# Kernel optimization log

Measured on AMD Instinct MI355X. Metric: run time of the kernel, lower is better.

## Reference

```python
import jax, jax.numpy as jnp
import numpy as np

M, H, D, P = 256, 32, 128, 4096
N = H * D
L = P + M  # total cache length after concat


def setup_inputs() -> dict:
    key = jax.random.key(0)
    ks = jax.random.split(key, 8)
    X = jax.random.normal(ks[0], (M, N), dtype=jnp.float32)
    # projection weights (nn.Linear stores [out, in]; y = x @ W.T)
    Wq = jax.random.normal(ks[1], (N, N), dtype=jnp.float32) * 0.005
    Wk = jax.random.normal(ks[2], (N, N), dtype=jnp.float32) * 0.005
    Wv = jax.random.normal(ks[3], (N, N), dtype=jnp.float32) * 0.005
    cache_K = jax.random.normal(ks[4], (H, P, D), dtype=jnp.float32) * 0.3
    cache_V = jax.random.normal(ks[5], (H, P, D), dtype=jnp.float32) * 0.3
    noise = jax.random.normal(ks[6], (H, M, L), dtype=jnp.float32) * 0.5
    tau = jnp.asarray(2.0, dtype=jnp.float32)
    return {"X": X, "Wq": Wq, "Wk": Wk, "Wv": Wv,
            "cache_K": cache_K, "cache_V": cache_V, "tau": tau, "noise": noise}


def reference(X, Wq, Wk, Wv, cache_K, cache_V, tau, noise):
    # project and split heads: [M, N] -> [H, M, D]
    q = (X @ Wq.T).reshape(M, H, D).transpose(1, 0, 2)
    k = (X @ Wk.T).reshape(M, H, D).transpose(1, 0, 2)
    v = (X @ Wv.T).reshape(M, H, D).transpose(1, 0, 2)
    k_cache = jnp.concatenate([cache_K, k], axis=1)  # [H, L, D]
    v_cache = jnp.concatenate([cache_V, v], axis=1)  # [H, L, D]
    c = jnp.einsum('hmd,hld->hml', q, k_cache)       # [H, M, L]
    # faithful to source: plain exp normalization (no max-subtract), twice
    c_exp = jnp.exp(c)
    c_exp_perturb = jnp.exp((c + noise) / tau)
    c_div = c_exp / jnp.sum(c_exp, axis=2, keepdims=True)
    c_div_perturb = c_exp_perturb / jnp.sum(c_exp_perturb, axis=2, keepdims=True)
    c_out = jnp.sum(c_div_perturb, axis=1)           # [H, L] token scores
    o = jnp.einsum('hml,hld->hmd', c_div, v_cache)   # [H, M, D]
    o2 = o.transpose(1, 0, 2).reshape(M, N)
    return o2, c_out
```

## Files before the change

kernel.cpp:

```cpp
#include <hip/hip_runtime.h>
#include <hip/hip_bf16.h>

#define MM 256
#define HH 32
#define DD 128
#define PP 4096
#define NN 4096
#define LL 4352
#define NSTR 8
#define SPL 4

typedef __attribute__((ext_vector_type(8))) short short8;
typedef __attribute__((ext_vector_type(4))) float f32x4;

__device__ __forceinline__ unsigned short f2bf(float f) {
    union { float f; unsigned u; } x; x.f = f;
    unsigned u = x.u;
    return (unsigned short)((u + 0x7fffu + ((u >> 16) & 1u)) >> 16);
}

__device__ __forceinline__ float bf2f(unsigned short u) {
    union { unsigned u; float f; } x; x.u = ((unsigned)u) << 16;
    return x.f;
}

__device__ __forceinline__ f32x4 mfma16(short8 a, short8 b, f32x4 c) {
    return __builtin_amdgcn_mfma_f32_16x16x32_bf16(a, b, c, 0, 0, 0);
}

__global__ __launch_bounds__(256) void conv_x_kernel(const float* __restrict__ src,
                                                     unsigned short* __restrict__ dst) {
    int i = blockIdx.x * 256 + threadIdx.x;
    long in0 = (long)i * 8;
    float4 f0 = *(const float4*)(src + in0);
    float4 f1 = *(const float4*)(src + in0 + 4);
    short8 v;
    v[0] = (short)f2bf(f0.x); v[1] = (short)f2bf(f0.y); v[2] = (short)f2bf(f0.z); v[3] = (short)f2bf(f0.w);
    v[4] = (short)f2bf(f1.x); v[5] = (short)f2bf(f1.y); v[6] = (short)f2bf(f1.z); v[7] = (short)f2bf(f1.w);
    *(short8*)(dst + in0) = v;
}

__global__ __launch_bounds__(256) void conv_k_kernel(const float* __restrict__ src,
                                                     unsigned short* __restrict__ dst) {
    int i = blockIdx.x * 256 + threadIdx.x;
    int h = i >> 16;
    long in0 = (long)i * 8;
    float4 f0 = *(const float4*)(src + in0);
    float4 f1 = *(const float4*)(src + in0 + 4);
    short8 v;
    v[0] = (short)f2bf(f0.x); v[1] = (short)f2bf(f0.y); v[2] = (short)f2bf(f0.z); v[3] = (short)f2bf(f0.w);
    v[4] = (short)f2bf(f1.x); v[5] = (short)f2bf(f1.y); v[6] = (short)f2bf(f1.z); v[7] = (short)f2bf(f1.w);
    *(short8*)(dst + in0 + (long)h * (LL - PP) * DD) = v;
}

__global__ __launch_bounds__(256) void conv_vt_kernel(const float* __restrict__ src,
                                                      unsigned short* __restrict__ dst) {
    __shared__ unsigned short tile[64][65];
    int h = blockIdx.z, l0 = blockIdx.x * 64, d0 = blockIdx.y * 64;
    int t = threadIdx.x;
    int r = t >> 2, c0 = (t & 3) * 16;
    const float* sp = src + ((long)h * PP + l0 + r) * DD + d0 + c0;
#pragma unroll
    for (int j = 0; j < 16; j += 4) {
        float4 f = *(const float4*)(sp + j);
        tile[r][c0 + j + 0] = f2bf(f.x); tile[r][c0 + j + 1] = f2bf(f.y);
        tile[r][c0 + j + 2] = f2bf(f.z); tile[r][c0 + j + 3] = f2bf(f.w);
    }
    __syncthreads();
    unsigned short* dp = dst + ((long)h * DD + d0 + r) * LL + l0 + c0;
    short8 o0, o1;
#pragma unroll
    for (int j = 0; j < 8; ++j) o0[j] = (short)tile[c0 + j][r];
#pragma unroll
    for (int j = 0; j < 8; ++j) o1[j] = (short)tile[c0 + 8 + j][r];
    *(short8*)(dp) = o0;
    *(short8*)(dp + 8) = o1;
}

__device__ __forceinline__ void proj_body(unsigned short* As, unsigned short* Bs,
    const unsigned short* __restrict__ xp, const float* __restrict__ wp,
    int& k0, bool guard, short8 (&ar)[4], float4& b0, float4& b1,
    int arow, int ak0, int brow, int bk0, int mo, int no, int lg, int li,
    f32x4 (&acc)[4][2]) {
#pragma unroll
    for (int c = 0; c < 4; ++c) {
        int kb = (ak0 + c * 8) * 2;
        *(short8*)((char*)As + arow * 128 + (kb ^ ((arow & 7) << 4))) = ar[c];
    }
    {
        short8 v;
        v[0] = (short)f2bf(b0.x); v[1] = (short)f2bf(b0.y); v[2] = (short)f2bf(b0.z); v[3] = (short)f2bf(b0.w);
        v[4] = (short)f2bf(b1.x); v[5] = (short)f2bf(b1.y); v[6] = (short)f2bf(b1.z); v[7] = (short)f2bf(b1.w);
        int kb = bk0 * 2;
        *(short8*)((char*)Bs + brow * 128 + (kb ^ ((brow & 7) << 4))) = v;
    }
    __syncthreads();
    if (guard) {
#pragma unroll
        for (int c = 0; c < 4; ++c) ar[c] = *(const short8*)(xp + k0 + 128 + c * 8);
        b0 = *(const float4*)(wp + k0 + 128);
        b1 = *(const float4*)(wp + k0 + 132);
    }
#pragma unroll
    for (int kk = 0; kk < 2; ++kk) {
        short8 a[4], b[2];
        int kb = kk * 64 + lg * 16;
#pragma unroll
        for (int i = 0; i < 4; ++i) {
            int row = mo + i * 16 + li;
            a[i] = *(const short8*)((char*)As + row * 128 + (kb ^ ((row & 7) << 4)));
        }
#pragma unroll
        for (int j = 0; j < 2; ++j) {
            int row = no + j * 16 + li;
            b[j] = *(const short8*)((char*)Bs + row * 128 + (kb ^ ((row & 7) << 4)));
        }
#pragma unroll
        for (int i = 0; i < 4; ++i)
#pragma unroll
            for (int j = 0; j < 2; ++j)
                acc[i][j] = mfma16(a[i], b[j], acc[i][j]);
    }
    __syncthreads();
    k0 += 64;
}

__global__ __launch_bounds__(512) void proj_gemm_kernel(const unsigned short* __restrict__ xb,
    const float* __restrict__ Wq, const float* __restrict__ Wk, const float* __restrict__ Wv,
    float* __restrict__ qkvfP) {
    const int widx = blockIdx.z;
    const float* __restrict__ W = (widx == 0) ? Wq : (widx == 1 ? Wk : Wv);
    const int n0 = blockIdx.x * 64;
    const int ks = blockIdx.y;
    __shared__ unsigned short As[256 * 64];
    __shared__ unsigned short Bs[64 * 64];
    const int t = threadIdx.x;
    const int wv = t >> 6, lane = t & 63;
    const int lg = lane >> 4, li = lane & 15;
    const int mo = (wv >> 1) * 64, no = (wv & 1) * 32;
    f32x4 acc[4][2];
#pragma unroll
    for (int i = 0; i < 4; ++i)
#pragma unroll
        for (int j = 0; j < 2; ++j) acc[i][j] = (f32x4){0.f, 0.f, 0.f, 0.f};

    const int arow = t >> 1, ak0 = (t & 1) * 32;
    const int brow = t >> 3, bk0 = (t & 7) * 8;
    const unsigned short* xp = xb + (long)arow * NN + ak0;
    const float* wp = W + (long)(n0 + brow) * NN + bk0;

    int k0 = ks * 1024;
    short8 aA[4], aB[4];
    float4 bA0, bA1, bB0, bB1;
#pragma unroll
    for (int c = 0; c < 4; ++c) aA[c] = *(const short8*)(xp + k0 + c * 8);
    bA0 = *(const float4*)(wp + k0);
    bA1 = *(const float4*)(wp + k0 + 4);
#pragma unroll
    for (int c = 0; c < 4; ++c) aB[c] = *(const short8*)(xp + k0 + 64 + c * 8);
    bB0 = *(const float4*)(wp + k0 + 64);
    bB1 = *(const float4*)(wp + k0 + 68);

    for (int it2 = 0; it2 < 8; ++it2) {
        const bool guard = (it2 < 7);
        proj_body(As, Bs, xp, wp, k0, guard, aA, bA0, bA1,
                  arow, ak0, brow, bk0, mo, no, lg, li, acc);
        proj_body(As, Bs, xp, wp, k0, guard, aB, bB0, bB1,
                  arow, ak0, brow, bk0, mo, no, lg, li, acc);
    }

    float* dst = qkvfP + ((long)ks * 3 + widx) * MM * NN;
#pragma unroll
    for (int i = 0; i < 4; ++i)
#pragma unroll
        for (int j = 0; j < 2; ++j)
#pragma unroll
            for (int r = 0; r < 4; ++r) {
                int m = mo + i * 16 + lg * 4 + r;
                int n = n0 + no + j * 16 + li;
                dst[(long)m * NN + n] = acc[i][j][r];
            }
}

__global__ __launch_bounds__(256) void epi_qk_kernel(const float* __restrict__ qkvfP,
    unsigned short* __restrict__ qb, unsigned short* __restrict__ kcat) {
    int i = blockIdx.x * 256 + threadIdx.x;
    int w = i >> 17;
    int r = i & 131071;
    int m = r >> 9;
    int n = (r & 511) * 8;
    float4 f0 = {0,0,0,0}, f1 = {0,0,0,0};
#pragma unroll
    for (int s = 0; s < SPL; ++s) {
        const float* sp = qkvfP + ((long)s * 3 + w) * MM * NN + (long)m * NN + n;
        float4 a0 = *(const float4*)(sp);
        float4 a1 = *(const float4*)(sp + 4);
        f0.x += a0.x; f0.y += a0.y; f0.z += a0.z; f0.w += a0.w;
        f1.x += a1.x; f1.y += a1.y; f1.z += a1.z; f1.w += a1.w;
    }
    short8 v;
    v[0]=(short)f2bf(f0.x); v[1]=(short)f2bf(f0.y); v[2]=(short)f2bf(f0.z); v[3]=(short)f2bf(f0.w);
    v[4]=(short)f2bf(f1.x); v[5]=(short)f2bf(f1.y); v[6]=(short)f2bf(f1.z); v[7]=(short)f2bf(f1.w);
    int h = n >> 7, d = n & 127;
    if (w == 0) *(short8*)(qb + ((long)h * MM + m) * DD + d) = v;
    else        *(short8*)(kcat + ((long)h * LL + PP + m) * DD + d) = v;
}

__global__ __launch_bounds__(256) void epi_v_kernel(const float* __restrict__ qkvfP,
    unsigned short* __restrict__ vT) {
    __shared__ unsigned short tile[64][65];
    int m0 = blockIdx.x * 64, n0 = blockIdx.y * 64;
    int t = threadIdx.x;
    int r = t >> 2, c0 = (t & 3) * 16;
#pragma unroll
    for (int j = 0; j < 16; j += 4) {
        float4 f = {0,0,0,0};
#pragma unroll
        for (int s = 0; s < SPL; ++s) {
            const float* sp = qkvfP + ((long)s * 3 + 2) * MM * NN + (long)(m0 + r) * NN + n0 + c0 + j;
            float4 a = *(const float4*)(sp);
            f.x += a.x; f.y += a.y; f.z += a.z; f.w += a.w;
        }
        tile[r][c0 + j + 0] = f2bf(f.x); tile[r][c0 + j + 1] = f2bf(f.y);
        tile[r][c0 + j + 2] = f2bf(f.z); tile[r][c0 + j + 3] = f2bf(f.w);
    }
    __syncthreads();
    int h = n0 >> 7, d0 = n0 & 127;
    unsigned short* dp = vT + ((long)h * DD + d0 + r) * LL + PP + m0 + c0;
    short8 o0, o1;
#pragma unroll
    for (int j = 0; j < 8; ++j) o0[j] = (short)tile[c0 + j][r];
#pragma unroll
    for (int j = 0; j < 8; ++j) o1[j] = (short)tile[c0 + 8 + j][r];
    *(short8*)(dp) = o0;
    *(short8*)(dp + 8) = o1;
}

__global__ __launch_bounds__(256) void attn_score_kernel(const unsigned short* __restrict__ qb,
    const unsigned short* __restrict__ kcat, const float* __restrict__ noise,
    const float* __restrict__ tau, float* __restrict__ S1, float* __restrict__ S2,
    unsigned short* __restrict__ e1b, unsigned short* __restrict__ e2b) {
    const int bid = blockIdx.x;
    const int swz = (bid & 7) * 272 + (bid >> 3);
    const int ls = swz % 17;
    const int mb = (swz / 17) & 3;
    const int h  = swz / 68;
    const int t = threadIdx.x, wv = t >> 6, lane = t & 63;
    const int lg = lane >> 4, li = lane & 15;
    __shared__ unsigned short kbuf[2][32][136];
    __shared__ float cs[64][36];
    const float inv_tau = 1.0f / tau[0];

    const int mA = mb * 64 + wv * 16 + li;
    const unsigned short* qp = qb + ((long)h * MM + mA) * DD + lg * 8;
    short8 aq[4];
#pragma unroll
    for (int dc = 0; dc < 4; ++dc) aq[dc] = *(const short8*)(qp + dc * 32);

    const int row_l = t >> 2;
    const int col0 = (t & 3) * 8;
    const int mrow_g = mb * 64 + row_l;
    const float* np = noise + ((long)h * MM + mrow_g) * LL + ls * 256 + col0;
    unsigned short* e1p = e1b + ((long)h * MM + mrow_g) * LL + ls * 256 + col0;
    unsigned short* e2p = e2b + ((long)h * MM + mrow_g) * LL + ls * 256 + col0;

    const int srow = t >> 3;
    const int scol = (t & 7) * 16;
    const unsigned short* ksrc = kcat + ((long)h * LL + ls * 256 + srow) * DD + scol;

    short8 s0 = *(const short8*)(ksrc);
    short8 s1 = *(const short8*)(ksrc + 8);
    *(short8*)(&kbuf[0][srow][scol]) = s0;
    *(short8*)(&kbuf[0][srow][scol + 8]) = s1;

    float4 nA0 = *(const float4*)(np);
    float4 nA1 = *(const float4*)(np + 4);
    float4 nB0 = *(const float4*)(np + 32);
    float4 nB1 = *(const float4*)(np + 36);

    float s1t = 0.f, s2t = 0.f;
    int cur = 0;
    __syncthreads();

    for (int lc = 0; lc < 8; ++lc) {
        if (lc < 7) {
            const unsigned short* p = ksrc + (long)((lc + 1) * 32) * DD;
            s0 = *(const short8*)(p);
            s1 = *(const short8*)(p + 8);
        }
        f32x4 c0 = (f32x4){0.f,0.f,0.f,0.f}, c1 = (f32x4){0.f,0.f,0.f,0.f};
#pragma unroll
        for (int dc = 0; dc < 4; ++dc) {
            short8 k0 = *(const short8*)(&kbuf[cur][li][dc * 32 + lg * 8]);
            short8 k1 = *(const short8*)(&kbuf[cur][16 + li][dc * 32 + lg * 8]);
            c0 = mfma16(aq[dc], k0, c0);
            c1 = mfma16(aq[dc], k1, c1);
        }
#pragma unroll
        for (int r = 0; r < 4; ++r) {
            cs[wv * 16 + lg * 4 + r][li] = c0[r];
            cs[wv * 16 + lg * 4 + r][16 + li] = c1[r];
        }
        float4 cva = *(const float4*)(&cs[row_l][col0]);
        float4 cvb = *(const float4*)(&cs[row_l][col0 + 4]);
        float cv[8] = {cva.x, cva.y, cva.z, cva.w, cvb.x, cvb.y, cvb.z, cvb.w};
        float nn[8] = {nA0.x, nA0.y, nA0.z, nA0.w, nA1.x, nA1.y, nA1.z, nA1.w};
        short8 v1, v2;
#pragma unroll
        for (int j = 0; j < 8; ++j) {
            float e1 = __expf(cv[j]);
            float e2 = __expf((cv[j] + nn[j]) * inv_tau);
            s1t += e1;
            s2t += e2;
            v1[j] = (short)f2bf(e1);
            v2[j] = (short)f2bf(e2);
        }
        *(short8*)(e1p + lc * 32) = v1;
        *(short8*)(e2p + lc * 32) = v2;
        nA0 = nB0; nA1 = nB1;
        int nx = (lc + 2 < 8) ? (lc + 2) : 7;
        nB0 = *(const float4*)(np + nx * 32);
        nB1 = *(const float4*)(np + nx * 32 + 4);
        if (lc < 7) {
            *(short8*)(&kbuf[cur ^ 1][srow][scol]) = s0;
            *(short8*)(&kbuf[cur ^ 1][srow][scol + 8]) = s1;
        }
        __syncthreads();
        cur ^= 1;
    }

    s1t += __shfl_xor(s1t, 1); s1t += __shfl_xor(s1t, 2);
    s2t += __shfl_xor(s2t, 1); s2t += __shfl_xor(s2t, 2);
    if ((t & 3) == 0) {
        atomicAdd(&S1[h * MM + mrow_g], s1t);
        atomicAdd(&S2[h * MM + mrow_g], s2t);
    }
}

__global__ __launch_bounds__(256) void attn_pv_kernel(const unsigned short* __restrict__ e1b,
    const unsigned short* __restrict__ vT, float* __restrict__ owsP) {
    const int bid = blockIdx.x;
    const int swz = (bid & 7) * 256 + (bid >> 3);
    const int ls = swz & 7;
    const int mb = (swz >> 3) & 3;
    const int dh = (swz >> 5) & 1;
    const int h  = swz >> 6;
    const int t = threadIdx.x, wv = t >> 6, lane = t & 63;
    const int lg = lane >> 4, li = lane & 15;
    __shared__ unsigned short vbuf[2][64][40];
    f32x4 acc[4];
#pragma unroll
    for (int df = 0; df < 4; ++df) acc[df] = (f32x4){0.f, 0.f, 0.f, 0.f};

    const unsigned short* pap = e1b + ((long)h * MM + mb * 64 + wv * 16 + li) * LL + ls * 544 + lg * 8;
    const int vrow = t >> 2, vcol = (t & 3) * 8;
    const unsigned short* vsrc = vT + ((long)h * DD + dh * 64 + vrow) * LL + ls * 544 + vcol;

    short8 vs = *(const short8*)(vsrc);
    *(short8*)(&vbuf[0][vrow][vcol]) = vs;
    short8 pa = __builtin_nontemporal_load((const short8*)(pap));
    int cur = 0;
    __syncthreads();

    for (int lc = 0; lc < 17; ++lc) {
        short8 pan;
        if (lc < 16) {
            vs = *(const short8*)(vsrc + (lc + 1) * 32);
            pan = __builtin_nontemporal_load((const short8*)(pap + (lc + 1) * 32));
        }
#pragma unroll
        for (int df = 0; df < 4; ++df) {
            short8 bv = *(const short8*)(&vbuf[cur][df * 16 + li][lg * 8]);
            acc[df] = mfma16(pa, bv, acc[df]);
        }
        if (lc < 16) {
            *(short8*)(&vbuf[cur ^ 1][vrow][vcol]) = vs;
            pa = pan;
        }
        __syncthreads();
        cur ^= 1;
    }

    const int mD = mb * 64 + wv * 16 + lg * 4;
    float* op = owsP + ((long)ls * HH + h) * MM * DD;
#pragma unroll
    for (int df = 0; df < 4; ++df)
#pragma unroll
        for (int r = 0; r < 4; ++r)
            op[(long)(mD + r) * DD + dh * 64 + df * 16 + li] = acc[df][r];
}

__global__ __launch_bounds__(256) void finalize_o_kernel(const float* __restrict__ owsP,
    const float* __restrict__ S1, const float* __restrict__ S2,
    float* __restrict__ out, float* __restrict__ invS2) {
    int i = blockIdx.x * 256 + threadIdx.x;
    int hm = i >> 5;
    int d4 = (i & 31) * 4;
    int h = hm >> 8, m = hm & 255;
    float4 s = {0,0,0,0};
#pragma unroll
    for (int st = 0; st < NSTR; ++st) {
        const float4 v = *(const float4*)(owsP + ((long)st * HH * MM + hm) * DD + d4);
        s.x += v.x; s.y += v.y; s.z += v.z; s.w += v.w;
    }
    float inv = 1.0f / S1[hm];
    float4 o;
    o.x = s.x * inv; o.y = s.y * inv; o.z = s.z * inv; o.w = s.w * inv;
    *(float4*)(out + (long)m * NN + h * DD + d4) = o;
    if ((i & 31) == 0) invS2[hm] = 1.0f / S2[hm];
}

__global__ __launch_bounds__(256) void attn_p2_kernel(const unsigned short* __restrict__ e2b,
    const float* __restrict__ invS2, float* __restrict__ cout) {
    const int h = blockIdx.y;
    const int l = blockIdx.x * 256 + threadIdx.x;
    const unsigned short* ep = e2b + (long)h * MM * LL + l;
    const float* is2 = invS2 + h * MM;
    float acc0 = 0.f, acc1 = 0.f, acc2 = 0.f, acc3 = 0.f;
    for (int m = 0; m < MM; m += 4) {
        acc0 += bf2f(__builtin_nontemporal_load(ep + (long)(m + 0) * LL)) * is2[m + 0];
        acc1 += bf2f(__builtin_nontemporal_load(ep + (long)(m + 1) * LL)) * is2[m + 1];
        acc2 += bf2f(__builtin_nontemporal_load(ep + (long)(m + 2) * LL)) * is2[m + 2];
        acc3 += bf2f(__builtin_nontemporal_load(ep + (long)(m + 3) * LL)) * is2[m + 3];
    }
    cout[(long)h * LL + l] = (acc0 + acc1) + (acc2 + acc3);
}

extern "C" void kernel_launch(void* const* d_in, const int* in_sizes, int n_in,
                              void* d_out, int out_size, void* d_ws, size_t ws_size,
                              hipStream_t stream) {
    const float* X     = (const float*)d_in[0];
    const float* Wq    = (const float*)d_in[1];
    const float* Wk    = (const float*)d_in[2];
    const float* Wv    = (const float*)d_in[3];
    const float* cK    = (const float*)d_in[4];
    const float* cV    = (const float*)d_in[5];
    const float* tau   = (const float*)d_in[6];
    const float* noise = (const float*)d_in[7];
    float* out = (float*)d_out;

    char* ws = (char*)d_ws;
    size_t off = 0;
    unsigned short* qb   = (unsigned short*)(ws + off); off += (size_t)HH * MM * DD * 2;
    unsigned short* kcat = (unsigned short*)(ws + off); off += (size_t)HH * LL * DD * 2;
    unsigned short* vT   = (unsigned short*)(ws + off); off += (size_t)HH * LL * DD * 2;
    float* S1    = (float*)(ws + off); off += (size_t)HH * MM * 4;
    float* S2    = (float*)(ws + off); off += (size_t)HH * MM * 4;
    float* invS2 = (float*)(ws + off); off += (size_t)HH * MM * 4;
    float* owsP  = (float*)(ws + off); off += (size_t)NSTR * HH * MM * DD * 4;
    size_t alias0 = off;
    unsigned short* xb = (unsigned short*)(ws + alias0);
    float* qkvfP = (float*)(ws + alias0 + (size_t)MM * NN * 2);
    unsigned short* e1b = (unsigned short*)(ws + alias0);
    off = alias0 + (size_t)HH * MM * LL * 2;
    unsigned short* e2b = (unsigned short*)(ws + off); off += (size_t)HH * MM * LL * 2;

    hipMemsetAsync(S1, 0, 2 * (size_t)HH * MM * 4, stream);

    conv_x_kernel<<<512, 256, 0, stream>>>(X, xb);
    conv_k_kernel<<<8192, 256, 0, stream>>>(cK, kcat);
    conv_vt_kernel<<<dim3(64, 2, 32), 256, 0, stream>>>(cV, vT);
    proj_gemm_kernel<<<dim3(64, SPL, 3), 512, 0, stream>>>(xb, Wq, Wk, Wv, qkvfP);
    epi_qk_kernel<<<1024, 256, 0, stream>>>(qkvfP, qb, kcat);
    epi_v_kernel<<<dim3(4, 64), 256, 0, stream>>>(qkvfP, vT);
    attn_score_kernel<<<2176, 256, 0, stream>>>(qb, kcat, noise, tau, S1, S2, e1b, e2b);
    attn_pv_kernel<<<2048, 256, 0, stream>>>(e1b, vT, owsP);
    finalize_o_kernel<<<1024, 256, 0, stream>>>(owsP, S1, S2, out, invS2);
    attn_p2_kernel<<<dim3(17, 32), 256, 0, stream>>>(e2b, invS2, out + (size_t)MM * NN);
}
```

Measured before the change: 299.9 us.

## Fuse score and PV kernels to keep exp(scores) tile in shared memory

Measured after the change: 247.2 us. 17.6% less time.

```diff
diff --git a/kernel.cpp b/kernel.cpp
--- a/kernel.cpp
+++ b/kernel.cpp
@@ -236,19 +236,22 @@
     *(short8*)(dp + 8) = o1;
 }
 
-__global__ __launch_bounds__(256) void attn_score_kernel(const unsigned short* __restrict__ qb,
-    const unsigned short* __restrict__ kcat, const float* __restrict__ noise,
-    const float* __restrict__ tau, float* __restrict__ S1, float* __restrict__ S2,
-    unsigned short* __restrict__ e1b, unsigned short* __restrict__ e2b) {
+__global__ __launch_bounds__(256) void attn_fused_kernel(const unsigned short* __restrict__ qb,
+    const unsigned short* __restrict__ kcat, const unsigned short* __restrict__ vT,
+    const float* __restrict__ noise, const float* __restrict__ tau,
+    float* __restrict__ S1, float* __restrict__ S2,
+    unsigned short* __restrict__ e2b, float* __restrict__ owsP) {
     const int bid = blockIdx.x;
-    const int swz = (bid & 7) * 272 + (bid >> 3);
-    const int ls = swz % 17;
-    const int mb = (swz / 17) & 3;
-    const int h  = swz / 68;
+    const int swz = (bid & 7) * 128 + (bid >> 3);
+    const int mb = swz & 3;
+    const int ls = (swz >> 2) & 7;
+    const int h  = swz >> 5;
     const int t = threadIdx.x, wv = t >> 6, lane = t & 63;
     const int lg = lane >> 4, li = lane & 15;
     __shared__ unsigned short kbuf[2][32][136];
+    __shared__ unsigned short vbuf[2][128][40];
     __shared__ float cs[64][36];
+    __shared__ unsigned short pbuf[64][40];
     const float inv_tau = 1.0f / tau[0];
 
     const int mA = mb * 64 + wv * 16 + li;
@@ -260,33 +263,45 @@
     const int row_l = t >> 2;
     const int col0 = (t & 3) * 8;
     const int mrow_g = mb * 64 + row_l;
-    const float* np = noise + ((long)h * MM + mrow_g) * LL + ls * 256 + col0;
-    unsigned short* e1p = e1b + ((long)h * MM + mrow_g) * LL + ls * 256 + col0;
-    unsigned short* e2p = e2b + ((long)h * MM + mrow_g) * LL + ls * 256 + col0;
-
-    const int srow = t >> 3;
-    const int scol = (t & 7) * 16;
-    const unsigned short* ksrc = kcat + ((long)h * LL + ls * 256 + srow) * DD + scol;
-
-    short8 s0 = *(const short8*)(ksrc);
-    short8 s1 = *(const short8*)(ksrc + 8);
-    *(short8*)(&kbuf[0][srow][scol]) = s0;
-    *(short8*)(&kbuf[0][srow][scol + 8]) = s1;
-
+    const float* np = noise + ((long)h * MM + mrow_g) * LL + ls * 544 + col0;
+    unsigned short* e2p = e2b + ((long)h * MM + mrow_g) * LL + ls * 544 + col0;
+
+    const int srow = t >> 3, scol = (t & 7) * 16;
+    const unsigned short* ksrc = kcat + ((long)h * LL + ls * 544 + srow) * DD + scol;
+    const int vrow = t >> 1, vcol = (t & 1) * 16;
+    const unsigned short* vsrc = vT + ((long)h * DD + vrow) * LL + ls * 544 + vcol;
+
+    {
+        short8 k0 = *(const short8*)(ksrc);
+        short8 k1 = *(const short8*)(ksrc + 8);
+        *(short8*)(&kbuf[0][srow][scol]) = k0;
+        *(short8*)(&kbuf[0][srow][scol + 8]) = k1;
+        short8 v0 = *(const short8*)(vsrc);
+        short8 v1 = *(const short8*)(vsrc + 8);
+        *(short8*)(&vbuf[0][vrow][vcol]) = v0;
+        *(short8*)(&vbuf[0][vrow][vcol + 8]) = v1;
+    }
     float4 nA0 = *(const float4*)(np);
     float4 nA1 = *(const float4*)(np + 4);
     float4 nB0 = *(const float4*)(np + 32);
     float4 nB1 = *(const float4*)(np + 36);
 
+    f32x4 acc[8];
+#pragma unroll
+    for (int dt = 0; dt < 8; ++dt) acc[dt] = (f32x4){0.f, 0.f, 0.f, 0.f};
     float s1t = 0.f, s2t = 0.f;
     int cur = 0;
     __syncthreads();
 
-    for (int lc = 0; lc < 8; ++lc) {
-        if (lc < 7) {
-            const unsigned short* p = ksrc + (long)((lc + 1) * 32) * DD;
-            s0 = *(const short8*)(p);
-            s1 = *(const short8*)(p + 8);
+    for (int lc = 0; lc < 17; ++lc) {
+        short8 kn0, kn1, vn0, vn1;
+        if (lc < 16) {
+            const unsigned short* pk = ksrc + (long)((lc + 1) * 32) * DD;
+            kn0 = *(const short8*)(pk);
+            kn1 = *(const short8*)(pk + 8);
+            const unsigned short* pv = vsrc + (lc + 1) * 32;
+            vn0 = *(const short8*)(pv);
+            vn1 = *(const short8*)(pv + 8);
         }
         f32x4 c0 = (f32x4){0.f,0.f,0.f,0.f}, c1 = (f32x4){0.f,0.f,0.f,0.f};
 #pragma unroll
@@ -315,15 +330,25 @@
             v1[j] = (short)f2bf(e1);
             v2[j] = (short)f2bf(e2);
         }
-        *(short8*)(e1p + lc * 32) = v1;
         *(short8*)(e2p + lc * 32) = v2;
+        *(short8*)(&pbuf[row_l][col0]) = v1;
         nA0 = nB0; nA1 = nB1;
-        int nx = (lc + 2 < 8) ? (lc + 2) : 7;
+        int nx = (lc + 2 < 17) ? (lc + 2) : 16;
         nB0 = *(const float4*)(np + nx * 32);
         nB1 = *(const float4*)(np + nx * 32 + 4);
-        if (lc < 7) {
-            *(short8*)(&kbuf[cur ^ 1][srow][scol]) = s0;
-            *(short8*)(&kbuf[cur ^ 1][srow][scol + 8]) = s1;
+        {
+            short8 pa = *(const short8*)(&pbuf[wv * 16 + li][lg * 8]);
+#pragma unroll
+            for (int dt = 0; dt < 8; ++dt) {
+                short8 bv = *(const short8*)(&vbuf[cur][dt * 16 + li][lg * 8]);
+                acc[dt] = mfma16(pa, bv, acc[dt]);
+            }
+        }
+        if (lc < 16) {
+            *(short8*)(&kbuf[cur ^ 1][srow][scol]) = kn0;
+            *(short8*)(&kbuf[cur ^ 1][srow][scol + 8]) = kn1;
+            *(short8*)(&vbuf[cur ^ 1][vrow][vcol]) = vn0;
+            *(short8*)(&vbuf[cur ^ 1][vrow][vcol + 8]) = vn1;
         }
         __syncthreads();
         cur ^= 1;
@@ -335,59 +360,14 @@
         atomicAdd(&S1[h * MM + mrow_g], s1t);
         atomicAdd(&S2[h * MM + mrow_g], s2t);
     }
-}
-
-__global__ __launch_bounds__(256) void attn_pv_kernel(const unsigned short* __restrict__ e1b,
-    const unsigned short* __restrict__ vT, float* __restrict__ owsP) {
-    const int bid = blockIdx.x;
-    const int swz = (bid & 7) * 256 + (bid >> 3);
-    const int ls = swz & 7;
-    const int mb = (swz >> 3) & 3;
-    const int dh = (swz >> 5) & 1;
-    const int h  = swz >> 6;
-    const int t = threadIdx.x, wv = t >> 6, lane = t & 63;
-    const int lg = lane >> 4, li = lane & 15;
-    __shared__ unsigned short vbuf[2][64][40];
-    f32x4 acc[4];
-#pragma unroll
-    for (int df = 0; df < 4; ++df) acc[df] = (f32x4){0.f, 0.f, 0.f, 0.f};
-
-    const unsigned short* pap = e1b + ((long)h * MM + mb * 64 + wv * 16 + li) * LL + ls * 544 + lg * 8;
-    const int vrow = t >> 2, vcol = (t & 3) * 8;
-    const unsigned short* vsrc = vT + ((long)h * DD + dh * 64 + vrow) * LL + ls * 544 + vcol;
-
-    short8 vs = *(const short8*)(vsrc);
-    *(short8*)(&vbuf[0][vrow][vcol]) = vs;
-    short8 pa = __builtin_nontemporal_load((const short8*)(pap));
-    int cur = 0;
-    __syncthreads();
-
-    for (int lc = 0; lc < 17; ++lc) {
-        short8 pan;
-        if (lc < 16) {
-            vs = *(const short8*)(vsrc + (lc + 1) * 32);
-            pan = __builtin_nontemporal_load((const short8*)(pap + (lc + 1) * 32));
-        }
-#pragma unroll
-        for (int df = 0; df < 4; ++df) {
-            short8 bv = *(const short8*)(&vbuf[cur][df * 16 + li][lg * 8]);
-            acc[df] = mfma16(pa, bv, acc[df]);
-        }
-        if (lc < 16) {
-            *(short8*)(&vbuf[cur ^ 1][vrow][vcol]) = vs;
-            pa = pan;
-        }
-        __syncthreads();
-        cur ^= 1;
-    }
 
     const int mD = mb * 64 + wv * 16 + lg * 4;
     float* op = owsP + ((long)ls * HH + h) * MM * DD;
 #pragma unroll
-    for (int df = 0; df < 4; ++df)
+    for (int dt = 0; dt < 8; ++dt)
 #pragma unroll
         for (int r = 0; r < 4; ++r)
-            op[(long)(mD + r) * DD + dh * 64 + df * 16 + li] = acc[df][r];
+            op[(long)(mD + r) * DD + dt * 16 + li] = acc[dt][r];
 }
 
 __global__ __launch_bounds__(256) void finalize_o_kernel(const float* __restrict__ owsP,
@@ -448,11 +428,8 @@
     float* S2    = (float*)(ws + off); off += (size_t)HH * MM * 4;
     float* invS2 = (float*)(ws + off); off += (size_t)HH * MM * 4;
     float* owsP  = (float*)(ws + off); off += (size_t)NSTR * HH * MM * DD * 4;
-    size_t alias0 = off;
-    unsigned short* xb = (unsigned short*)(ws + alias0);
-    float* qkvfP = (float*)(ws + alias0 + (size_t)MM * NN * 2);
-    unsigned short* e1b = (unsigned short*)(ws + alias0);
-    off = alias0 + (size_t)HH * MM * LL * 2;
+    unsigned short* xb = (unsigned short*)(ws + off); off += (size_t)MM * NN * 2;
+    float* qkvfP = (float*)(ws + off); off += (size_t)SPL * 3 * MM * NN * 4;
     unsigned short* e2b = (unsigned short*)(ws + off); off += (size_t)HH * MM * LL * 2;
 
     hipMemsetAsync(S1, 0, 2 * (size_t)HH * MM * 4, stream);
@@ -463,8 +440,7 @@
     proj_gemm_kernel<<<dim3(64, SPL, 3), 512, 0, stream>>>(xb, Wq, Wk, Wv, qkvfP);
     epi_qk_kernel<<<1024, 256, 0, stream>>>(qkvfP, qb, kcat);
     epi_v_kernel<<<dim3(4, 64), 256, 0, stream>>>(qkvfP, vT);
-    attn_score_kernel<<<2176, 256, 0, stream>>>(qb, kcat, noise, tau, S1, S2, e1b, e2b);
-    attn_pv_kernel<<<2048, 256, 0, stream>>>(e1b, vT, owsP);
+    attn_fused_kernel<<<1024, 256, 0, stream>>>(qb, kcat, vT, noise, tau, S1, S2, e2b, owsP);
     finalize_o_kernel<<<1024, 256, 0, stream>>>(owsP, S1, S2, out, invS2);
     attn_p2_kernel<<<dim3(17, 32), 256, 0, stream>>>(e2b, invS2, out + (size_t)MM * NN);
 }
```
